# Performance work log

Hardware: AMD Instinct MI355X
Metric: run time of the kernel (lower is better)

## Reference

```python
import jax, jax.numpy as jnp
import numpy as np

B, L, C, H, Wd = 256, 64, 256, 32, 32  # batch, num_filts, code_dim, height, width

def setup_inputs() -> dict:
    key = jax.random.key(0)
    k1, k2 = jax.random.split(key)
    code = jax.random.normal(k1, (B, L, C), dtype=jnp.float32)
    # stacked per-filter weights: weights[l].weight has shape [code_dim, H*W]
    W = jax.random.normal(k2, (L, C, H * Wd), dtype=jnp.float32) * (1.0 / np.sqrt(C))
    return {"code": code, "W": W}

def reference(code, W):
    # Original: for each filter l, x_hat[:, l] = code[:, l, :] @ weights[l].weight
    # (F.linear(x, weight.t()) == x @ weight). Fuse into one batched GEMM.
    # code: [B, L, C], W: [L, C, HW] -> out: [B, L, HW]
    x_hat = jnp.einsum('blc,lcd->bld', code, W)
    return x_hat.reshape(code.shape[0], W.shape[0], H, Wd)
```

## Files before the change

kernel.cpp:

```cpp
#include <hip/hip_runtime.h>
#include <hip/hip_bf16.h>

#define B_  256
#define L_  64
#define C_  256
#define HW_ 1024

typedef float  floatx4 __attribute__((ext_vector_type(4)));
typedef __bf16 bf16x8  __attribute__((ext_vector_type(8)));
typedef __bf16 bf16x4  __attribute__((ext_vector_type(4)));

#define LDT 72

#define BARRIER_LDS() asm volatile("s_waitcnt lgkmcnt(0)\n\ts_barrier" ::: "memory")

__global__ __launch_bounds__(512, 4)
void gld_mfma_kernel(const float* __restrict__ code,
                     const float* __restrict__ W,
                     float* __restrict__ out)
{
    const int tid = threadIdx.x;
    const int l   = blockIdx.z;
    const int m0  = blockIdx.y * 128;
    const int n0  = blockIdx.x * 128;

    __shared__ __bf16 Alds[128 * LDT];
    __shared__ __bf16 Blds[128 * LDT];

    const int lane = tid & 63;
    const int wave = tid >> 6;
    const int wm = (wave >> 2) * 64;
    const int wn = (wave & 3) * 32;

    floatx4 acc[4][2];
    #pragma unroll
    for (int i = 0; i < 4; ++i)
        #pragma unroll
        for (int j = 0; j < 2; ++j)
            acc[i][j] = (floatx4)0.0f;

    const int a_row = tid >> 4;
    const int a_kc  = (tid & 15) * 4;
    const int b_nt = (tid & 31) * 4;
    const int b_kt = (tid >> 5) * 4;

    const float* aBase = code + (size_t)m0 * (L_ * C_) + (size_t)l * C_ + a_kc;
    const float* wBase = W + (size_t)l * (C_ * HW_) + (size_t)b_kt * HW_ + n0 + b_nt;

    floatx4 Areg[4], Breg[4];

    #pragma unroll
    for (int p = 0; p < 4; ++p)
        Areg[p] = *(const floatx4*)(aBase + (size_t)(p * 32 + a_row) * (L_ * C_));
    #pragma unroll
    for (int i = 0; i < 4; ++i)
        Breg[i] = *(const floatx4*)(wBase + (size_t)i * HW_);

    #pragma unroll
    for (int kb = 0; kb < C_; kb += 64) {
        #pragma unroll
        for (int p = 0; p < 4; ++p) {
            bf16x4 h;
            h.x = (__bf16)Areg[p].x; h.y = (__bf16)Areg[p].y;
            h.z = (__bf16)Areg[p].z; h.w = (__bf16)Areg[p].w;
            *(bf16x4*)&Alds[(p * 32 + a_row) * LDT + a_kc] = h;
        }
        #pragma unroll
        for (int j = 0; j < 4; ++j) {
            bf16x4 h;
            h.x = (__bf16)Breg[0][j]; h.y = (__bf16)Breg[1][j];
            h.z = (__bf16)Breg[2][j]; h.w = (__bf16)Breg[3][j];
            *(bf16x4*)&Blds[(b_nt + j) * LDT + b_kt] = h;
        }

        if (kb + 64 < C_) {
            #pragma unroll
            for (int p = 0; p < 4; ++p)
                Areg[p] = *(const floatx4*)(aBase + (size_t)(p * 32 + a_row) * (L_ * C_) + (kb + 64));
            #pragma unroll
            for (int i = 0; i < 4; ++i)
                Breg[i] = *(const floatx4*)(wBase + (size_t)(kb + 64 + i) * HW_);
        }

        BARRIER_LDS();

        #pragma unroll
        for (int ks = 0; ks < 2; ++ks) {
            bf16x8 af[4], bfr[2];
            const int koff = ks * 32 + (lane >> 4) * 8;
            #pragma unroll
            for (int i = 0; i < 4; ++i)
                af[i] = *(const bf16x8*)&Alds[(wm + i * 16 + (lane & 15)) * LDT + koff];
            #pragma unroll
            for (int j = 0; j < 2; ++j)
                bfr[j] = *(const bf16x8*)&Blds[(wn + j * 16 + (lane & 15)) * LDT + koff];
            #pragma unroll
            for (int i = 0; i < 4; ++i)
                #pragma unroll
                for (int j = 0; j < 2; ++j)
                    acc[i][j] = __builtin_amdgcn_mfma_f32_16x16x32_bf16(af[i], bfr[j], acc[i][j], 0, 0, 0);
        }

        BARRIER_LDS();
    }

    const int col0 = lane & 15;
    const int row0 = (lane >> 4) * 4;
    #pragma unroll
    for (int i = 0; i < 4; ++i) {
        #pragma unroll
        for (int j = 0; j < 2; ++j) {
            const int m = m0 + wm + i * 16 + row0;
            const int n = n0 + wn + j * 16 + col0;
            float* o = out + (size_t)m * (L_ * HW_) + (size_t)l * HW_ + n;
            #pragma unroll
            for (int r = 0; r < 4; ++r)
                o[(size_t)r * (L_ * HW_)] = acc[i][j][r];
        }
    }
}

extern "C" void kernel_launch(void* const* d_in, const int* in_sizes, int n_in,
                              void* d_out, int out_size, void* d_ws, size_t ws_size,
                              hipStream_t stream) {
    const float* code = (const float*)d_in[0];
    const float* W    = (const float*)d_in[1];
    float* out        = (float*)d_out;

    dim3 grid(HW_ / 128, B_ / 128, L_);
    gld_mfma_kernel<<<grid, 512, 0, stream>>>(code, W, out);
}
```

Before: 140.9 us.

## Prefetch W tiles two stages ahead and skew B LDS writes by lane

The W (B operand) global loads are now double-buffered in registers and issued two K-blocks ahead instead of one, to hide more global memory latency. The k-quad each thread loads is rotated by (group+lane)&15, which spreads the transposed bf16 writes into Blds across LDS banks to reduce bank conflicts. This costs 16 extra VGPRs per thread under a 512-thread, 4-block launch bound, which could cause spills or lower occupancy.

Measured after the change: 149.0 us. 1.06x slower.

```diff
diff --git a/kernel.cpp b/kernel.cpp
--- a/kernel.cpp
+++ b/kernel.cpp
@@ -41,23 +41,37 @@
 
     const int a_row = tid >> 4;
     const int a_kc  = (tid & 15) * 4;
-    const int b_nt = (tid & 31) * 4;
-    const int b_kt = (tid >> 5) * 4;
+    const int b_i  = tid & 31;
+    const int b_g  = tid >> 5;
+    const int b_kq = (b_g + b_i) & 15;
 
     const float* aBase = code + (size_t)m0 * (L_ * C_) + (size_t)l * C_ + a_kc;
-    const float* wBase = W + (size_t)l * (C_ * HW_) + (size_t)b_kt * HW_ + n0 + b_nt;
+    const float* wBase = W + (size_t)l * (C_ * HW_) + n0 + 4 * b_i;
 
-    floatx4 Areg[4], Breg[4];
+    floatx4 Areg[4];
+    floatx4 Breg[2][4];
 
     #pragma unroll
     for (int p = 0; p < 4; ++p)
         Areg[p] = *(const floatx4*)(aBase + (size_t)(p * 32 + a_row) * (L_ * C_));
     #pragma unroll
-    for (int i = 0; i < 4; ++i)
-        Breg[i] = *(const floatx4*)(wBase + (size_t)i * HW_);
+    for (int r = 0; r < 4; ++r)
+        Breg[0][r] = *(const floatx4*)(wBase + (size_t)(4 * b_kq + r) * HW_);
+    #pragma unroll
+    for (int r = 0; r < 4; ++r)
+        Breg[1][r] = *(const floatx4*)(wBase + (size_t)(64 + 4 * b_kq + r) * HW_);
 
     #pragma unroll
     for (int kb = 0; kb < C_; kb += 64) {
+        const int pb = (kb >> 6) & 1;
+
+        #pragma unroll
+        for (int j = 0; j < 4; ++j) {
+            bf16x4 h;
+            h.x = (__bf16)Breg[pb][0][j]; h.y = (__bf16)Breg[pb][1][j];
+            h.z = (__bf16)Breg[pb][2][j]; h.w = (__bf16)Breg[pb][3][j];
+            *(bf16x4*)&Blds[(4 * b_i + j) * LDT + 4 * b_kq] = h;
+        }
         #pragma unroll
         for (int p = 0; p < 4; ++p) {
             bf16x4 h;
@@ -65,21 +79,16 @@
             h.z = (__bf16)Areg[p].z; h.w = (__bf16)Areg[p].w;
             *(bf16x4*)&Alds[(p * 32 + a_row) * LDT + a_kc] = h;
         }
-        #pragma unroll
-        for (int j = 0; j < 4; ++j) {
-            bf16x4 h;
-            h.x = (__bf16)Breg[0][j]; h.y = (__bf16)Breg[1][j];
-            h.z = (__bf16)Breg[2][j]; h.w = (__bf16)Breg[3][j];
-            *(bf16x4*)&Blds[(b_nt + j) * LDT + b_kt] = h;
-        }
 
         if (kb + 64 < C_) {
             #pragma unroll
             for (int p = 0; p < 4; ++p)
                 Areg[p] = *(const floatx4*)(aBase + (size_t)(p * 32 + a_row) * (L_ * C_) + (kb + 64));
+        }
+        if (kb + 128 < C_) {
             #pragma unroll
-            for (int i = 0; i < 4; ++i)
-                Breg[i] = *(const floatx4*)(wBase + (size_t)(kb + 64 + i) * HW_);
+            for (int r = 0; r < 4; ++r)
+                Breg[pb][r] = *(const floatx4*)(wBase + (size_t)(kb + 128 + 4 * b_kq + r) * HW_);
         }
 
         BARRIER_LDS();
```
